# Performance work log

Hardware: AMD Instinct MI355X
Metric: run time of the kernel (lower is better)

Reference implementation:

```python
import jax, jax.numpy as jnp
import numpy as np

DIM = 96
HEADS = 4
HID = int(DIM * 2.66)  # 255, GDFN hidden width
B, H, W = 4, 128, 128


def _conv(x, w, b=None, groups=1):
    y = jax.lax.conv_general_dilated(x, w, (1, 1), 'SAME',
                                     dimension_numbers=('NCHW', 'OIHW', 'NCHW'),
                                     feature_group_count=groups)
    return y if b is None else y + b[None, :, None, None]


def _ln(x, w, b):
    # WithBias LayerNorm over channel dim (per pixel), biased variance, eps=1e-5
    mu = x.mean(1, keepdims=True)
    var = ((x - mu) ** 2).mean(1, keepdims=True)
    return (x - mu) / jnp.sqrt(var + 1e-5) * w[None, :, None, None] + b[None, :, None, None]


def _l2norm(x):
    # torch F.normalize(dim=-1): x / max(||x||_2, 1e-12)
    return x / jnp.maximum(jnp.linalg.norm(x, axis=-1, keepdims=True), 1e-12)


def _gelu(x):
    return jax.nn.gelu(x, approximate=False)


def setup_inputs() -> dict:
    key = jax.random.key(0)
    ks = iter(jax.random.split(key, 32))
    nrm = lambda shp, s=0.02: jax.random.normal(next(ks), shp, dtype=jnp.float32) * s
    d, h2 = DIM, HID
    inp = {
        'x': jax.random.normal(next(ks), (B, DIM, H, W), dtype=jnp.float32),
        # L_conv: 3x3(d->d,+b) GELU 1x1(d->1,+b)
        'Lc_w1': nrm((d, d, 3, 3)), 'Lc_b1': jnp.zeros((d,), jnp.float32),
        'Lc_w2': nrm((1, d, 1, 1)), 'Lc_b2': jnp.zeros((1,), jnp.float32),
        # R_conv: 3x3(d->d,+b) GELU 1x1(d->3,+b)
        'Rc_w1': nrm((d, d, 3, 3)), 'Rc_b1': jnp.zeros((d,), jnp.float32),
        'Rc_w2': nrm((3, d, 1, 1)), 'Rc_b2': jnp.zeros((3,), jnp.float32),
        # L_rein: 3x3(1->d,+b) GELU ; R_rein: 3x3(3->d,+b)
        'Lr_w': nrm((d, 1, 3, 3)), 'Lr_b': jnp.zeros((d,), jnp.float32),
        'Rr_w': nrm((d, 3, 3, 3)), 'Rr_b': jnp.zeros((d,), jnp.float32),
        # LayerNorms (WithBias)
        'n1_w': jnp.ones((d,), jnp.float32), 'n1_b': jnp.zeros((d,), jnp.float32),
        'nL_w': jnp.ones((d,), jnp.float32), 'nL_b': jnp.zeros((d,), jnp.float32),
        'n2_w': jnp.ones((d,), jnp.float32), 'n2_b': jnp.zeros((d,), jnp.float32),
        # Illum_Attention (bias=False)
        'temp': jnp.ones((HEADS, 1, 1), jnp.float32),
        'q_w': nrm((d, d, 1, 1)),
        'qd_w': nrm((d, d, 3, 3)),          # q_dwconv is a FULL 3x3 conv (no groups)
        'kv_w': nrm((2 * d, d, 1, 1)),
        'kvd_w': nrm((2 * d, 1, 3, 3)),     # depthwise, groups=2*dim
        'po_w': nrm((d, d, 1, 1)),
        # FeedForward (bias=False); NOTE: 'dwconv' here is a FULL 3x3 conv
        'pi_w': nrm((h2, d, 1, 1)),
        'fdw_w': nrm((h2, h2, 3, 3)),
        'fpo_w': nrm((d, h2, 1, 1)),
    }
    return inp


def reference(x, Lc_w1, Lc_b1, Lc_w2, Lc_b2, Rc_w1, Rc_b1, Rc_w2, Rc_b2,
              Lr_w, Lr_b, Rr_w, Rr_b, n1_w, n1_b, nL_w, nL_b, n2_w, n2_b,
              temp, q_w, qd_w, kv_w, kvd_w, po_w, pi_w, fdw_w, fpo_w):
    b, c, h, w = x.shape
    # Retinex decomposition heads
    L = _conv(_gelu(_conv(x, Lc_w1, Lc_b1)), Lc_w2, Lc_b2)   # [b,1,h,w]
    R = _conv(_gelu(_conv(x, Rc_w1, Rc_b1)), Rc_w2, Rc_b2)   # [b,3,h,w]
    L_rein = _gelu(_conv(jax.lax.stop_gradient(L), Lr_w, Lr_b))  # detach in torch
    R_rein = _conv(jax.lax.stop_gradient(R), Rr_w, Rr_b)
    # Illum_Guided_TransformerBlock: x = x + attn(norm1(x), normL(illum))
    xn = _ln(x, n1_w, n1_b)
    ill = _ln(L_rein, nL_w, nL_b)
    q = _conv(_conv(ill, q_w), qd_w)
    kv = _conv(_conv(xn, kv_w), kvd_w, groups=2 * c)
    k, v = jnp.split(kv, 2, axis=1)
    ch, hw = c // HEADS, h * w
    heads = lambda t: t.reshape(b, HEADS, ch, hw)
    qh, kh, vh = _l2norm(heads(q)), _l2norm(heads(k)), heads(v)
    # channel-wise attention: [b,heads,ch,ch]
    attn = jax.nn.softmax(jnp.einsum('bhci,bhdi->bhcd', qh, kh) * temp[None], axis=-1)
    out = jnp.einsum('bhcd,bhdi->bhci', attn, vh).reshape(b, c, h, w)
    x = x + _conv(out, po_w)
    # x = x + ffn(norm2(x))
    x2 = _ln(x, n2_w, n2_b)
    x = x + _conv(_gelu(_conv(_conv(x2, pi_w), fdw_w)), fpo_w)
    x = x + R_rein
    return (x, L, R)
```

## Files before the change

### kernel.cpp

```cpp
#include <hip/hip_runtime.h>

#define HWsz 16384
#define Wd 128

typedef unsigned short ushortT;
typedef unsigned int uintT;
typedef __attribute__((ext_vector_type(8))) short short8v;
typedef __attribute__((ext_vector_type(4))) float f32x4;
typedef __attribute__((ext_vector_type(16))) float f32x16;
typedef __attribute__((ext_vector_type(4))) unsigned short ushort4v;

__device__ __forceinline__ float gelu_f(float x){
    return 0.5f * x * (1.0f + erff(x * 0.70710678118654752f));
}
__device__ __forceinline__ ushortT f2b(float f){
    union { float f; uintT u; } v; v.f = f;
    uintT r = v.u + 0x7FFFu + ((v.u >> 16) & 1u);
    return (ushortT)(r >> 16);
}
__device__ __forceinline__ float b2f(ushortT u){
    union { uintT u; float f; } v; v.u = ((uintT)u) << 16; return v.f;
}

__device__ __forceinline__ void pack3_one(int e, const float* __restrict__ w,
    ushortT* __restrict__ outp, int cout, int cin, int BN, int NCH)
{
    int j = e & 7; int r = e >> 3;
    int ocl = r % BN; r /= BN;
    int kg  = r & 3;  r >>= 2;
    int tap = r % 9;  r /= 9;
    int ch  = r % NCH;
    int nt  = r / NCH;
    int ci = ch*32 + kg*8 + j;
    int oc = nt*BN + ocl;
    float v = (oc < cout && ci < cin) ? w[((size_t)oc*cin + ci)*9 + tap] : 0.f;
    outp[e] = f2b(v);
}
__device__ __forceinline__ void pack1_one(int e, const float* __restrict__ w,
    ushortT* __restrict__ outp, int cout, int cin, int BN, int NCH)
{
    int j = e & 7; int r = e >> 3;
    int ocl = r % BN; r /= BN;
    int kg  = r & 3;  r >>= 2;
    int ch  = r % NCH;
    int nt  = r / NCH;
    int ci = ch*32 + kg*8 + j;
    int oc = nt*BN + ocl;
    float v = (oc < cout && ci < cin) ? w[(size_t)oc*cin + ci] : 0.f;
    outp[e] = f2b(v);
}
__global__ __launch_bounds__(256) void pack_all_kernel(
    const float* Lc, const float* Rc, const float* Qd, const float* Fd,
    const float* Q1, const float* KV1, const float* PI1, const float* FPO1,
    ushortT* dL, ushortT* dR, ushortT* dQ, ushortT* dF,
    ushortT* dq0, ushortT* dkv, ushortT* dpi, ushortT* dfpo)
{
    int e = blockIdx.x*256 + threadIdx.x;
    if      (e < 82944)  pack3_one(e,        Lc, dL, 96, 96, 48, 3);
    else if (e < 165888) pack3_one(e-82944,  Rc, dR, 96, 96, 48, 3);
    else if (e < 248832) pack3_one(e-165888, Qd, dQ, 96, 96, 32, 3);
    else if (e < 838656) pack3_one(e-248832, Fd, dF, 255,255, 64, 8);
    else if (e < 847872) pack1_one(e-838656, Q1, dq0, 96, 96, 96, 3);
    else if (e < 866304) pack1_one(e-847872, KV1,dkv, 192,96, 48, 3);
    else if (e < 890880) pack1_one(e-866304, PI1,dpi, 255,96, 64, 3);
    else if (e < 915456) pack1_one(e-890880, FPO1,dfpo,96,255, 96, 8);
}

__global__ __launch_bounds__(256) void tonhwc_kernel(
    const float* __restrict__ in, ushortT* __restrict__ outp)
{
    const int p = blockIdx.x*256 + threadIdx.x;
    const int b = blockIdx.y;
    const float* ip = in + (size_t)b*96*HWsz + p;
    ushortT* op = outp + ((size_t)b*HWsz + p)*96;
#pragma unroll
    for (int g=0; g<12; g++){
        float v[8];
#pragma unroll
        for (int c=0;c<8;c++) v[c] = ip[(size_t)(g*8+c)*HWsz];
        uint4 pk;
        pk.x = (uintT)f2b(v[0]) | ((uintT)f2b(v[1])<<16);
        pk.y = (uintT)f2b(v[2]) | ((uintT)f2b(v[3])<<16);
        pk.z = (uintT)f2b(v[4]) | ((uintT)f2b(v[5])<<16);
        pk.w = (uintT)f2b(v[6]) | ((uintT)f2b(v[7])<<16);
        *(uint4*)(op + g*8) = pk;
    }
}

template<int NG, int NCH, int ACT, int TWOOUT>
__global__ __launch_bounds__(256,3) void conv3x3_v3(
    const ushortT* __restrict__ inh,
    const ushortT* __restrict__ wpk1, const ushortT* __restrict__ wpk2,
    const float* __restrict__ bias1, const float* __restrict__ bias2,
    ushortT* __restrict__ out1, ushortT* __restrict__ out2,
    int cout, int ocpad)
{
    constexpr int BN = NG*16;
    constexpr int Cpad = NCH*32;
    constexpr int WCH = 9*4*BN*8;
    __shared__ __align__(16) ushortT As[4*180*8];
    __shared__ __align__(16) ushortT Ws[WCH];

    const int tid = threadIdx.x;
    const int l   = tid & 63;
    const int wv  = tid >> 6;
    const int l15 = l & 15;
    const int kg  = l >> 4;
    const int tix = blockIdx.x & 7, tiy = blockIdx.x >> 3;
    const int b   = blockIdx.z;
    const int x0 = tix*16, y0 = tiy*8;

    int nt = blockIdx.y;
    const ushortT* wpk; const float* bias; ushortT* outp; int ntw;
    if (TWOOUT && nt >= 2){ wpk = wpk2; bias = bias2; outp = out2; ntw = nt-2; }
    else { wpk = wpk1; bias = bias1; outp = out1; ntw = nt; }
    const int ocbase = ntw*BN;

    f32x4 acc[2][NG];
#pragma unroll
    for (int m=0;m<2;m++)
#pragma unroll
        for (int n=0;n<NG;n++) acc[m][n] = (f32x4){0.f,0.f,0.f,0.f};

    const ushortT* inb = inh + (size_t)b*HWsz*Cpad;

    for (int ch=0; ch<NCH; ch++){
        __syncthreads();
        if (tid < 180){
            int hy = tid/18, hx = tid - hy*18;
            int gy = y0 + hy - 1, gx = x0 + hx - 1;
            bool ok = ((unsigned)gy < 128u) && ((unsigned)gx < 128u);
#pragma unroll
            for (int g=0; g<4; g++){
                uint4 v; v.x=0u; v.y=0u; v.z=0u; v.w=0u;
                if (ok) v = *(const uint4*)(inb + (size_t)(gy*Wd+gx)*Cpad + ch*32 + g*8);
                *(uint4*)(As + (g*180+tid)*8) = v;
            }
        }
        {
            const uint4* wsrc = (const uint4*)(wpk + ((size_t)ntw*NCH + ch)*WCH);
            uint4* wdst = (uint4*)Ws;
            for (int t=tid; t<WCH/8; t+=256) wdst[t] = wsrc[t];
        }
        __syncthreads();
#pragma unroll
        for (int tp=0; tp<9; tp++){
            const int dy = tp/3, dx = tp - dy*3;
            short8v bf[NG];
#pragma unroll
            for (int n=0;n<NG;n++)
                bf[n] = *(const short8v*)(Ws + ((size_t)(tp*4 + kg)*BN + n*16 + l15)*8);
#pragma unroll
            for (int mg=0;mg<2;mg++){
                short8v a = *(const short8v*)(As + (kg*180 + (wv*2+mg+dy)*18 + l15+dx)*8);
#pragma unroll
                for (int n=0;n<NG;n++)
                    acc[mg][n] = __builtin_amdgcn_mfma_f32_16x16x32_bf16(a, bf[n], acc[mg][n], 0,0,0);
            }
        }
    }
    __syncthreads();
    ushortT* Ts = As + wv*1024;
#pragma unroll
    for (int mg=0;mg<2;mg++){
        int gy = y0 + wv*2 + mg;
        ushortT* orow = outp + ((size_t)b*HWsz + gy*Wd + x0)*ocpad + ocbase;
#pragma unroll
        for (int n=0;n<NG;n++){
            int ocl = n*16 + l15;
            int oc  = ocbase + ocl;
            float bs = (bias && oc < cout) ? bias[oc] : 0.f;
#pragma unroll
            for (int j=0;j<4;j++){
                int pxj = kg*4 + j;
                float r = 0.f;
                if (oc < cout){ r = acc[mg][n][j] + bs; if (ACT) r = gelu_f(r); }
                int seg = ((ocl>>3) + pxj) & 7;
                Ts[pxj*64 + seg*8 + (ocl&7)] = f2b(r);
            }
        }
#pragma unroll
        for (int ps=0; ps < (BN+31)/32; ps++){
            int rpx = l & 15;
            int rs  = (l>>4) + ps*4;
            if (rs*8 < BN){
                int pseg = (rs + rpx) & 7;
                short8v v = *(const short8v*)(Ts + rpx*64 + pseg*8);
                *(short8v*)(orow + (size_t)rpx*ocpad + rs*8) = v;
            }
        }
    }
}

template<int NGW, int NCH>
__global__ __launch_bounds__(256) void gemm1x1_v2(
    const ushortT* __restrict__ inh, const ushortT* __restrict__ wpk,
    ushortT* __restrict__ outp, int cout, int ocpad)
{
    constexpr int BN = NGW*16;
    constexpr int Cpad = NCH*32;
    __shared__ __align__(16) ushortT Ts[4*16*64];

    const int tid = threadIdx.x;
    const int l = tid & 63, wv = tid >> 6, l15 = l & 15, kg = l >> 4;
    const int p0 = blockIdx.x*64;
    const int b  = blockIdx.z;
    const int nt = wv, ocbase = wv*BN;
    const ushortT* inb = inh + (size_t)b*HWsz*Cpad;

    f32x4 acc[4][NGW];
#pragma unroll
    for (int m=0;m<4;m++)
#pragma unroll
        for (int n=0;n<NGW;n++) acc[m][n] = (f32x4){0.f,0.f,0.f,0.f};

#pragma unroll
    for (int ch=0; ch<NCH; ch++){
        short8v a[4], bw[NGW];
#pragma unroll
        for (int mg=0; mg<4; mg++)
            a[mg] = *(const short8v*)(inb + (size_t)(p0 + mg*16 + l15)*Cpad + ch*32 + kg*8);
#pragma unroll
        for (int n=0;n<NGW;n++)
            bw[n] = *(const short8v*)(wpk + (((size_t)(nt*NCH + ch)*4 + kg)*BN + n*16 + l15)*8);
#pragma unroll
        for (int mg=0;mg<4;mg++)
#pragma unroll
            for (int n=0;n<NGW;n++)
                acc[mg][n] = __builtin_amdgcn_mfma_f32_16x16x32_bf16(a[mg], bw[n], acc[mg][n], 0,0,0);
    }
    ushortT* Tw = Ts + wv*1024;
#pragma unroll
    for (int mg=0;mg<4;mg++){
        ushortT* orow = outp + ((size_t)b*HWsz + p0 + mg*16)*ocpad + ocbase;
#pragma unroll
        for (int n=0;n<NGW;n++){
            int ocl = n*16 + l15;
            int oc  = ocbase + ocl;
#pragma unroll
            for (int j=0;j<4;j++){
                int pxj = kg*4 + j;
                float r = (oc < cout) ? acc[mg][n][j] : 0.f;
                int seg = ((ocl>>3) + pxj) & 7;
                Tw[pxj*64 + seg*8 + (ocl&7)] = f2b(r);
            }
        }
#pragma unroll
        for (int ps=0; ps < (BN+31)/32; ps++){
            int rpx = l & 15;
            int rs  = (l>>4) + ps*4;
            if (rs*8 < BN){
                int pseg = (rs + rpx) & 7;
                short8v v = *(const short8v*)(Tw + rpx*64 + pseg*8);
                *(short8v*)(orow + (size_t)rpx*ocpad + rs*8) = v;
            }
        }
    }
}

template<int NG, int NCH, int ACT, int OMODE, int NSPLIT, int XMAP>
__global__ __launch_bounds__(256,4) void conv3x3_mfma(
    const ushortT* __restrict__ inh,
    const ushortT* __restrict__ wpk1, const ushortT* __restrict__ wpk2,
    const float* __restrict__ bias1, const float* __restrict__ bias2,
    void* __restrict__ out1, void* __restrict__ out2,
    int cout, int ocpad)
{
    constexpr int BN = NG*16;
    constexpr int Cpad = NCH*32;
    __shared__ __align__(16) ushortT As[4*324*8];

    const int tid = threadIdx.x;
    const int l   = tid & 63;
    const int wv  = tid >> 6;
    const int l15 = l & 15;
    const int kg  = l >> 4;
    int tile = blockIdx.x, nt = blockIdx.y, b = blockIdx.z;
    const int tix = tile & 7, tiy = tile >> 3;

    const ushortT* wpk = wpk1; const float* bias = bias1; void* outv = out1;
    if (NSPLIT > 0 && nt >= NSPLIT){ nt -= NSPLIT; wpk = wpk2; bias = bias2; outv = out2; }

    f32x4 acc[4][NG];
#pragma unroll
    for (int m=0;m<4;m++)
#pragma unroll
        for (int n=0;n<NG;n++) acc[m][n] = (f32x4){0.f,0.f,0.f,0.f};

    const ushortT* inb = inh + (size_t)b*HWsz*Cpad;

    for (int ch=0; ch<NCH; ch++){
        __syncthreads();
#pragma unroll
        for (int g=0; g<4; g++){
            for (int p=tid; p<324; p+=256){
                int hy = p/18, hx = p - hy*18;
                int gy = tiy*16 + hy - 1, gx = tix*16 + hx - 1;
                uint4 v; v.x=0u; v.y=0u; v.z=0u; v.w=0u;
                if ((unsigned)gy < 128u && (unsigned)gx < 128u)
                    v = *(const uint4*)(inb + (size_t)(gy*Wd+gx)*Cpad + ch*32 + g*8);
                *(uint4*)(As + (g*324+p)*8) = v;
            }
        }
        __syncthreads();
        const ushortT* wch = wpk + (size_t)(nt*NCH + ch)*(9*4*BN*8);
#pragma unroll
        for (int tp=0; tp<9; tp++){
            const int dy = tp/3, dx = tp - dy*3;
            short8v a[4], bf[NG];
#pragma unroll
            for (int mg=0; mg<4; mg++){
                int p = (wv*4 + mg + dy)*18 + l15 + dx;
                a[mg] = *(const short8v*)(As + (kg*324 + p)*8);
            }
#pragma unroll
            for (int n=0;n<NG;n++)
                bf[n] = *(const short8v*)(wch + ((size_t)(tp*4 + kg)*BN + n*16 + l15)*8);
#pragma unroll
            for (int mg=0;mg<4;mg++)
#pragma unroll
                for (int n=0;n<NG;n++)
                    acc[mg][n] = __builtin_amdgcn_mfma_f32_16x16x32_bf16(a[mg], bf[n], acc[mg][n], 0,0,0);
        }
    }
    if (OMODE == 2){
        ushortT* out = (ushortT*)outv;
#pragma unroll
        for (int n=0;n<NG;n++){
            int oc = nt*BN + n*16 + l15;
            if (oc < cout){
                float bs = bias ? bias[oc] : 0.f;
#pragma unroll
                for (int mg=0;mg<4;mg++){
                    int gy = tiy*16 + wv*4 + mg;
                    int gx = tix*16 + kg*4;
                    ushort4v pk;
#pragma unroll
                    for (int j=0;j<4;j++){
                        float r = acc[mg][n][j] + bs;
                        if (ACT) r = gelu_f(r);
                        pk[j] = f2b(r);
                    }
                    *(ushort4v*)(out + ((size_t)b*cout + oc)*HWsz + gy*Wd + gx) = pk;
                }
            }
        }
    }
}

template<int NG, int NCH, int RES, int OMODE, int XMAP>
__global__ __launch_bounds__(256) void gemm1x1_mfma(
    const ushortT* __restrict__ inh, const ushortT* __restrict__ wpk, int wstride_z,
    const float* __restrict__ res1, const ushortT* __restrict__ res2b,
    void* __restrict__ outv, int cout, int ocpad)
{
    constexpr int BN = NG*16;
    constexpr int Cpad = NCH*32;
    constexpr int LSTR = (BN <= 64) ? 64 : 128;
    constexpr int MASK = LSTR/8 - 1;
    __shared__ __align__(16) ushortT TsS[(OMODE==1) ? 4*16*LSTR : 16];

    const int tid = threadIdx.x;
    const int l = tid & 63, wv = tid >> 6, l15 = l & 15, kg = l >> 4;
    int chunk = blockIdx.x, nt = blockIdx.y, b = blockIdx.z;
    const int p0 = chunk*256 + wv*64;
    const ushortT* inb = inh + (size_t)b*HWsz*Cpad;
    const ushortT* wp  = wpk + (size_t)b*wstride_z;

    f32x4 acc[4][NG];
#pragma unroll
    for (int m=0;m<4;m++)
#pragma unroll
        for (int n=0;n<NG;n++) acc[m][n] = (f32x4){0.f,0.f,0.f,0.f};

#pragma unroll
    for (int ch=0; ch<NCH; ch++){
        short8v a[4], bw[NG];
#pragma unroll
        for (int mg=0; mg<4; mg++)
            a[mg] = *(const short8v*)(inb + (size_t)(p0 + mg*16 + l15)*Cpad + ch*32 + kg*8);
#pragma unroll
        for (int n=0;n<NG;n++)
            bw[n] = *(const short8v*)(wp + (((size_t)(nt*NCH + ch)*4 + kg)*BN + n*16 + l15)*8);
#pragma unroll
        for (int mg=0;mg<4;mg++)
#pragma unroll
            for (int n=0;n<NG;n++)
                acc[mg][n] = __builtin_amdgcn_mfma_f32_16x16x32_bf16(a[mg], bw[n], acc[mg][n], 0,0,0);
    }
    if (OMODE == 0){
        float* out = (float*)outv;
#pragma unroll
        for (int n=0;n<NG;n++){
            int oc = nt*BN + n*16 + l15;
            if (oc < cout){
#pragma unroll
                for (int mg=0;mg<4;mg++){
                    int pix = p0 + mg*16 + kg*4;
                    size_t idx = ((size_t)b*cout + oc)*HWsz + pix;
                    float4 r;
                    r.x = acc[mg][n][0]; r.y = acc[mg][n][1];
                    r.z = acc[mg][n][2]; r.w = acc[mg][n][3];
                    if (RES>=1){ float4 q = *(const float4*)(res1+idx); r.x+=q.x;r.y+=q.y;r.z+=q.z;r.w+=q.w; }
                    if (RES>=2){
                        ushort4v q = *(const ushort4v*)(res2b+idx);
                        r.x+=b2f(q[0]); r.y+=b2f(q[1]); r.z+=b2f(q[2]); r.w+=b2f(q[3]);
                    }
                    *(float4*)(out + idx) = r;
                }
            }
        }
    } else {
        ushortT* outp = (ushortT*)outv;
        ushortT* Ts = TsS + wv*(16*LSTR);
#pragma unroll
        for (int mg=0;mg<4;mg++){
            ushortT* orow = outp + ((size_t)b*HWsz + p0 + mg*16)*ocpad + nt*BN;
#pragma unroll
            for (int n=0;n<NG;n++){
                int ocl = n*16 + l15;
                int oc  = nt*BN + ocl;
#pragma unroll
                for (int j=0;j<4;j++){
                    int pxj = kg*4 + j;
                    float r = (oc < cout) ? acc[mg][n][j] : 0.f;
                    int seg = ((ocl>>3) + pxj) & MASK;
                    Ts[pxj*LSTR + seg*8 + (ocl&7)] = f2b(r);
                }
            }
#pragma unroll
            for (int ps=0; ps < (BN+31)/32; ps++){
                int rpx = l & 15;
                int rs  = (l>>4) + ps*4;
                if (rs*8 < BN){
                    int pseg = (rs + rpx) & MASK;
                    short8v v = *(const short8v*)(Ts + rpx*LSTR + pseg*8);
                    *(short8v*)(orow + (size_t)rpx*ocpad + rs*8) = v;
                }
            }
        }
    }
}

template<int NOUT>
__global__ __launch_bounds__(256) void head1x1_kernel(
    const ushortT* __restrict__ inh, const float* __restrict__ w,
    const float* __restrict__ bias, float* __restrict__ out)
{
    __shared__ float lw[NOUT*96];
    const int tid = threadIdx.x;
    for (int t=tid; t<NOUT*96; t+=256) lw[t] = w[t];
    __syncthreads();
    const int p = blockIdx.x*256 + tid;
    const int b = blockIdx.y;
    const ushortT* ip = inh + ((size_t)b*HWsz + p)*96;
    float v[96];
#pragma unroll
    for (int g=0; g<12; g++){
        short8v s = *(const short8v*)(ip + g*8);
#pragma unroll
        for (int i=0;i<8;i++) v[g*8+i] = b2f((ushortT)s[i]);
    }
#pragma unroll
    for (int oc=0; oc<NOUT; oc++){
        float acc = bias[oc];
#pragma unroll
        for (int c=0;c<96;c++) acc += v[c]*lw[oc*96+c];
        out[((size_t)b*NOUT + oc)*HWsz + p] = acc;
    }
}

__global__ __launch_bounds__(256) void lrein_ln_kernel(
    const float* __restrict__ L, const float* __restrict__ w,
    const float* __restrict__ bias, const float* __restrict__ lnw,
    const float* __restrict__ lnb, ushortT* __restrict__ outh)
{
    __shared__ float sw[864], sb[96], sn1[96], sn2[96];
    const int tid = threadIdx.x;
    for (int t=tid; t<864; t+=256) sw[t] = w[t];
    if (tid < 96){ sb[tid]=bias[tid]; sn1[tid]=lnw[tid]; sn2[tid]=lnb[tid]; }
    __syncthreads();
    const int p = blockIdx.x*256 + tid;
    const int b = blockIdx.y;
    const int y = p>>7, x = p&127;
    const float* ib = L + (size_t)b*HWsz;
    float win[9];
#pragma unroll
    for (int dy=0;dy<3;dy++)
#pragma unroll
        for (int dx=0;dx<3;dx++){
            int gy=y+dy-1, gx=x+dx-1;
            win[dy*3+dx] = ((unsigned)gy<128u && (unsigned)gx<128u) ? ib[gy*Wd+gx] : 0.f;
        }
    float v[96]; float s=0.f;
#pragma unroll
    for (int c=0;c<96;c++){
        float a = sb[c];
#pragma unroll
        for (int t=0;t<9;t++) a += win[t]*sw[c*9+t];
        a = gelu_f(a);
        v[c]=a; s+=a;
    }
    const float mu = s*(1.f/96.f);
    float s2=0.f;
#pragma unroll
    for (int c=0;c<96;c++){ float d=v[c]-mu; s2+=d*d; }
    const float inv = 1.f/sqrtf(s2*(1.f/96.f)+1e-5f);
    ushortT* op = outh + ((size_t)b*HWsz + p)*96;
#pragma unroll
    for (int g=0; g<12; g++){
        uint4 pk; uintT w4[4];
#pragma unroll
        for (int i=0;i<4;i++){
            float r0 = (v[g*8+2*i]-mu)*inv*sn1[g*8+2*i]+sn2[g*8+2*i];
            float r1 = (v[g*8+2*i+1]-mu)*inv*sn1[g*8+2*i+1]+sn2[g*8+2*i+1];
            w4[i] = (uintT)f2b(r0) | ((uintT)f2b(r1)<<16);
        }
        pk.x=w4[0]; pk.y=w4[1]; pk.z=w4[2]; pk.w=w4[3];
        *(uint4*)(op + g*8) = pk;
    }
}

__global__ __launch_bounds__(256) void ln_n2n_kernel(
    const float* __restrict__ in, const float* __restrict__ w,
    const float* __restrict__ bias, ushortT* __restrict__ outh)
{
    const int p = blockIdx.x*256+threadIdx.x;
    const int b = blockIdx.y;
    const float* ip = in + (size_t)b*96*HWsz + p;
    float v[96]; float s=0.f;
#pragma unroll
    for(int c=0;c<96;c++){ v[c]=ip[(size_t)c*HWsz]; s+=v[c]; }
    const float mu = s*(1.f/96.f);
    float s2=0.f;
#pragma unroll
    for(int c=0;c<96;c++){ float d=v[c]-mu; s2+=d*d; }
    const float inv = 1.f/sqrtf(s2*(1.f/96.f)+1e-5f);
    ushortT* op = outh + ((size_t)b*HWsz + p)*96;
#pragma unroll
    for (int g=0; g<12; g++){
        uint4 pk; uintT w4[4];
#pragma unroll
        for (int i=0;i<4;i++){
            float r0 = (v[g*8+2*i]-mu)*inv*w[g*8+2*i]+bias[g*8+2*i];
            float r1 = (v[g*8+2*i+1]-mu)*inv*w[g*8+2*i+1]+bias[g*8+2*i+1];
            w4[i] = (uintT)f2b(r0) | ((uintT)f2b(r1)<<16);
        }
        pk.x=w4[0]; pk.y=w4[1]; pk.z=w4[2]; pk.w=w4[3];
        *(uint4*)(op + g*8) = pk;
    }
}

__global__ __launch_bounds__(256) void conv3x3_rr_kernel(
    const float* __restrict__ in, const float* __restrict__ w,
    const float* __restrict__ bias, ushortT* __restrict__ out)
{
    __shared__ float sw[216], sb[8];
    const int oc0 = blockIdx.y*8;
    if (threadIdx.x < 216) sw[threadIdx.x] = w[(size_t)oc0*27 + threadIdx.x];
    if (threadIdx.x < 8)   sb[threadIdx.x] = bias[oc0 + threadIdx.x];
    __syncthreads();
    const int p = blockIdx.x*256+threadIdx.x;
    const int b = blockIdx.z;
    const int y=p>>7, x=p&127;
    const float* ib = in + (size_t)b*3*HWsz;
    float win[27];
#pragma unroll
    for (int ci=0;ci<3;ci++)
#pragma unroll
        for (int dy=0;dy<3;dy++)
#pragma unroll
            for (int dx=0;dx<3;dx++){
                int gy=y+dy-1, gx=x+dx-1;
                win[ci*9+dy*3+dx] = ((unsigned)gy<128u && (unsigned)gx<128u)
                    ? ib[(size_t)ci*HWsz + gy*Wd+gx] : 0.f;
            }
#pragma unroll
    for (int i=0;i<8;i++){
        float acc = sb[i];
#pragma unroll
        for (int t=0;t<27;t++) acc += win[t]*sw[i*27+t];
        out[((size_t)b*96 + oc0+i)*HWsz + p] = f2b(acc);
    }
}

__global__ __launch_bounds__(256) void dw_nhwc_kernel(
    const ushortT* __restrict__ inh, const float* __restrict__ w,
    ushortT* __restrict__ kout, ushortT* __restrict__ vouth)
{
    const int p = blockIdx.x*256+threadIdx.x;
    const int c0 = blockIdx.y*8;
    const int b = blockIdx.z;
    const int y=p>>7, x=p&127;
    float lw[72];
#pragma unroll
    for (int i=0;i<8;i++)
#pragma unroll
        for (int t=0;t<9;t++) lw[i*9+t] = w[(size_t)(c0+i)*9 + t];
    const ushortT* ib = inh + (size_t)b*HWsz*192;
    float acc[8];
#pragma unroll
    for (int i=0;i<8;i++) acc[i]=0.f;
#pragma unroll
    for(int dy=0;dy<3;dy++){
        int gy=y+dy-1;
        if((unsigned)gy<128u){
#pragma unroll
            for(int dx=0;dx<3;dx++){
                int gx=x+dx-1;
                if((unsigned)gx<128u){
                    short8v s = *(const short8v*)(ib + (size_t)(gy*Wd+gx)*192 + c0);
#pragma unroll
                    for (int i=0;i<8;i++) acc[i] += b2f((ushortT)s[i])*lw[i*9+dy*3+dx];
                }
            }
        }
    }
    if (c0 < 96){
#pragma unroll
        for (int i=0;i<8;i++)
            kout[((size_t)b*96 + c0+i)*HWsz + p] = f2b(acc[i]);
    } else {
        ushortT* op = vouth + ((size_t)b*HWsz + p)*96 + (c0-96);
        uint4 pk;
        pk.x = (uintT)f2b(acc[0]) | ((uintT)f2b(acc[1])<<16);
        pk.y = (uintT)f2b(acc[2]) | ((uintT)f2b(acc[3])<<16);
        pk.z = (uintT)f2b(acc[4]) | ((uintT)f2b(acc[5])<<16);
        pk.w = (uintT)f2b(acc[6]) | ((uintT)f2b(acc[7])<<16);
        *(uint4*)op = pk;
    }
}

__global__ __launch_bounds__(256) void rownorm_bf16_kernel(
    const ushortT* __restrict__ qb, const ushortT* __restrict__ kb,
    float* __restrict__ invqk)
{
    __shared__ float red[256];
    const int r = blockIdx.x;
    const ushortT* ip = (r < 384) ? (qb + (size_t)r*HWsz) : (kb + (size_t)(r-384)*HWsz);
    float s=0.f;
    const ushortT* tp = ip + threadIdx.x*64;
#pragma unroll
    for (int g=0; g<8; g++){
        short8v v = *(const short8v*)(tp + g*8);
#pragma unroll
        for (int i=0;i<8;i++){ float f = b2f((ushortT)v[i]); s += f*f; }
    }
    red[threadIdx.x]=s; __syncthreads();
    for(int st=128; st>0; st>>=1){
        if(threadIdx.x<st) red[threadIdx.x]+=red[threadIdx.x+st];
        __syncthreads();
    }
    if(threadIdx.x==0) invqk[r] = 1.f/fmaxf(sqrtf(red[0]), 1e-12f);
}

__global__ __launch_bounds__(256) void qk_mfma_kernel(
    const ushortT* __restrict__ qb, const ushortT* __restrict__ kb,
    float* __restrict__ part)
{
    const int tid = threadIdx.x;
    const int l = tid & 63, wv = tid >> 6;
    const int chunk = blockIdx.x*4 + wv;
    const int bh = blockIdx.y, b = bh>>2, h = bh&3;
    const int ch = min(l & 31, 23);
    const int kh = (l >> 5)*8;
    const ushortT* qp = qb + ((size_t)b*96 + h*24 + ch)*HWsz + chunk*512 + kh;
    const ushortT* kp = kb + ((size_t)b*96 + h*24 + ch)*HWsz + chunk*512 + kh;
    f32x16 acc;
#pragma unroll
    for (int r=0;r<16;r++) acc[r]=0.f;
    for (int ks=0; ks<32; ks++){
        short8v a  = *(const short8v*)(qp + ks*16);
        short8v bb = *(const short8v*)(kp + ks*16);
        acc = __builtin_amdgcn_mfma_f32_32x32x16_bf16(a, bb, acc, 0,0,0);
    }
    float* op = part + ((size_t)chunk*16 + bh)*1024;
    const int col = l & 31;
#pragma unroll
    for (int r=0;r<16;r++){
        int row = (r&3) + 8*(r>>2) + 4*(l>>5);
        op[row*32 + col] = acc[r];
    }
}

__global__ void qk_reduce_kernel(const float* __restrict__ part, float* __restrict__ out)
{
    int idx = blockIdx.x*256+threadIdx.x;
    float s=0.f;
    for(int c=0;c<32;c++) s += part[(size_t)c*16384 + idx];
    out[idx]=s;
}

__global__ __launch_bounds__(576) void softmax_kernel(
    const float* __restrict__ raw, const float* __restrict__ invq,
    const float* __restrict__ invk, const float* __restrict__ temp,
    float* __restrict__ attn)
{
    __shared__ float l[576];
    const int bh=blockIdx.x, b=bh>>2, h=bh&3;
    const int tid=threadIdx.x;
    const int i=tid/24, j=tid-i*24;
    l[tid] = raw[(size_t)bh*1024 + i*32 + j] * invq[b*96+h*24+i] * invk[b*96+h*24+j] * temp[h];
    __syncthreads();
    if(tid<24){
        float m=-1e30f;
#pragma unroll
        for(int jj=0;jj<24;jj++) m = fmaxf(m, l[tid*24+jj]);
        float e[24]; float s=0.f;
#pragma unroll
        for(int jj=0;jj<24;jj++){ e[jj]=__expf(l[tid*24+jj]-m); s+=e[jj]; }
        float isv = 1.f/s;
#pragma unroll
        for(int jj=0;jj<24;jj++) attn[(size_t)bh*576 + tid*24 + jj] = e[jj]*isv;
    }
}

__global__ __launch_bounds__(256) void mkM_kernel(
    const float* __restrict__ attn, const float* __restrict__ po_w,
    ushortT* __restrict__ Mpk)
{
    const int b = blockIdx.x;
    for (int e = threadIdx.x; e < 9216; e += 256){
        int oc = e / 96, d = e - oc*96;
        int h = d / 24, dl = d - h*24;
        const float* aw = attn + ((size_t)(b*4+h))*576 + dl;
        const float* pw = po_w + (size_t)oc*96 + h*24;
        float s = 0.f;
#pragma unroll
        for (int c=0;c<24;c++) s += pw[c]*aw[c*24];
        int ch = d>>5, kg = (d>>3)&3, j = d&7;
        Mpk[(size_t)b*9216 + ((size_t)(ch*4+kg)*96 + oc)*8 + j] = f2b(s);
    }
}

extern "C" void kernel_launch(void* const* d_in, const int* in_sizes, int n_in,
                              void* d_out, int out_size, void* d_ws, size_t ws_size,
                              hipStream_t stream)
{
    const float* x     = (const float*)d_in[0];
    const float* Lc_w1 = (const float*)d_in[1];
    const float* Lc_b1 = (const float*)d_in[2];
    const float* Lc_w2 = (const float*)d_in[3];
    const float* Lc_b2 = (const float*)d_in[4];
    const float* Rc_w1 = (const float*)d_in[5];
    const float* Rc_b1 = (const float*)d_in[6];
    const float* Rc_w2 = (const float*)d_in[7];
    const float* Rc_b2 = (const float*)d_in[8];
    const float* Lr_w  = (const float*)d_in[9];
    const float* Lr_b  = (const float*)d_in[10];
    const float* Rr_w  = (const float*)d_in[11];
    const float* Rr_b  = (const float*)d_in[12];
    const float* n1_w  = (const float*)d_in[13];
    const float* n1_b  = (const float*)d_in[14];
    const float* nL_w  = (const float*)d_in[15];
    const float* nL_b  = (const float*)d_in[16];
    const float* n2_w  = (const float*)d_in[17];
    const float* n2_b  = (const float*)d_in[18];
    const float* temp  = (const float*)d_in[19];
    const float* q_w   = (const float*)d_in[20];
    const float* qd_w  = (const float*)d_in[21];
    const float* kv_w  = (const float*)d_in[22];
    const float* kvd_w = (const float*)d_in[23];
    const float* po_w  = (const float*)d_in[24];
    const float* pi_w  = (const float*)d_in[25];
    const float* fdw_w = (const float*)d_in[26];
    const float* fpo_w = (const float*)d_in[27];

    char* base = (char*)d_ws;
    ushortT* xh   = (ushortT*)(base + 0);
    ushortT* f0h  = (ushortT*)(base + 0);
    ushortT* Lh   = (ushortT*)(base + 33554432);
    ushortT* kv0h = (ushortT*)(base + 33554432);
    ushortT* f1h  = (ushortT*)(base + 33554432);
    ushortT* Rh   = (ushortT*)(base + 67108864);
    ushortT* vh   = (ushortT*)(base + 67108864);
    ushortT* x2nh = (ushortT*)(base + 67108864);
    ushortT* illh = (ushortT*)(base + 79691776);
    ushortT* xnh  = (ushortT*)(base + 92274688);
    ushortT* q0h  = (ushortT*)(base + 104857600);
    ushortT* qb   = (ushortT*)(base + 117440512);
    float*   x1   = (float*)(base + 117440512);
    ushortT* kb   = (ushortT*)(base + 142606336);
    ushortT* Bb   = (ushortT*)(base + 155189248);
    char* smb = base + 167772160;
    ushortT* wpkL = (ushortT*)smb;   smb += 165888;
    ushortT* wpkR = (ushortT*)smb;   smb += 165888;
    ushortT* wpkQ = (ushortT*)smb;   smb += 165888;
    ushortT* wpkF = (ushortT*)smb;   smb += 1179648;
    ushortT* wq0  = (ushortT*)smb;   smb += 18432;
    ushortT* wkv  = (ushortT*)smb;   smb += 36864;
    ushortT* wpi  = (ushortT*)smb;   smb += 49152;
    ushortT* wfpo = (ushortT*)smb;   smb += 49152;
    ushortT* Mpk  = (ushortT*)smb;   smb += 73728;
    float* invqk  = (float*)smb;     smb += 3072;
    float* part   = (float*)smb;     smb += 2097152;
    float* araw   = (float*)smb;     smb += 65536;
    float* attn   = (float*)smb;     smb += 36864;

    float* out_x = (float*)d_out;
    float* out_L = out_x + (size_t)4*96*HWsz;
    float* out_R = out_L + (size_t)4*HWsz;

    dim3 blk(256);

    hipLaunchKernelGGL(pack_all_kernel, dim3(3576), blk, 0, stream,
        Lc_w1, Rc_w1, qd_w, fdw_w, q_w, kv_w, pi_w, fpo_w,
        wpkL, wpkR, wpkQ, wpkF, wq0, wkv, wpi, wfpo);
    hipLaunchKernelGGL(tonhwc_kernel, dim3(64,4), blk, 0, stream, x, xh);

    hipLaunchKernelGGL((conv3x3_v3<3,3,1,1>), dim3(128,4,4), blk, 0, stream,
        xh, wpkL, wpkR, Lc_b1, Rc_b1, Lh, Rh, 96, 96);
    hipLaunchKernelGGL((head1x1_kernel<1>), dim3(64,4), blk, 0, stream, Lh, Lc_w2, Lc_b2, out_L);
    hipLaunchKernelGGL((head1x1_kernel<3>), dim3(64,4), blk, 0, stream, Rh, Rc_w2, Rc_b2, out_R);
    hipLaunchKernelGGL(lrein_ln_kernel, dim3(64,4), blk, 0, stream, out_L, Lr_w, Lr_b, nL_w, nL_b, illh);
    hipLaunchKernelGGL(conv3x3_rr_kernel, dim3(64,12,4), blk, 0, stream, out_R, Rr_w, Rr_b, Bb);

    hipLaunchKernelGGL(ln_n2n_kernel, dim3(64,4), blk, 0, stream, x, n1_w, n1_b, xnh);

    hipLaunchKernelGGL((gemm1x1_mfma<6,3,0,1,0>), dim3(64,1,4), blk, 0, stream,
        illh, wq0, 0, nullptr, nullptr, (void*)q0h, 96, 96);
    hipLaunchKernelGGL((conv3x3_mfma<2,3,0,2,0,0>), dim3(64,3,4), blk, 0, stream,
        q0h, wpkQ, wpkQ, nullptr, nullptr, (void*)qb, (void*)qb, 96, 0);
    hipLaunchKernelGGL((gemm1x1_v2<3,3>), dim3(256,1,4), blk, 0, stream,
        xnh, wkv, kv0h, 192, 192);
    hipLaunchKernelGGL(dw_nhwc_kernel, dim3(64,24,4), blk, 0, stream, kv0h, kvd_w, kb, vh);

    hipLaunchKernelGGL(rownorm_bf16_kernel, dim3(768), blk, 0, stream, qb, kb, invqk);
    hipLaunchKernelGGL(qk_mfma_kernel, dim3(8,16), blk, 0, stream, qb, kb, part);
    hipLaunchKernelGGL(qk_reduce_kernel, dim3(64), blk, 0, stream, part, araw);
    hipLaunchKernelGGL(softmax_kernel, dim3(16), dim3(576), 0, stream, araw, invqk, invqk+384, temp, attn);
    hipLaunchKernelGGL(mkM_kernel, dim3(4), blk, 0, stream, attn, po_w, Mpk);
    hipLaunchKernelGGL((gemm1x1_mfma<6,3,1,0,0>), dim3(64,1,4), blk, 0, stream,
        vh, Mpk, 9216, x, nullptr, (void*)x1, 96, 0);

    hipLaunchKernelGGL(ln_n2n_kernel, dim3(64,4), blk, 0, stream, x1, n2_w, n2_b, x2nh);
    hipLaunchKernelGGL((gemm1x1_v2<4,3>), dim3(256,1,4), blk, 0, stream,
        x2nh, wpi, f0h, 255, 256);
    hipLaunchKernelGGL((conv3x3_v3<4,8,1,0>), dim3(128,4,4), blk, 0, stream,
        f0h, wpkF, wpkF, nullptr, nullptr, f1h, f1h, 255, 256);
    hipLaunchKernelGGL((gemm1x1_mfma<6,8,2,0,0>), dim3(64,1,4), blk, 0, stream,
        f1h, wfpo, 0, x1, Bb, (void*)out_x, 96, 0);
}
```

Measured before the change: 408.6 us.

## Double conv3x3 spatial tile height and load weights via direct global-to-LDS

```diff
diff --git a/kernel.cpp b/kernel.cpp
--- a/kernel.cpp
+++ b/kernel.cpp
@@ -20,6 +20,11 @@
 }
 __device__ __forceinline__ float b2f(ushortT u){
     union { uintT u; float f; } v; v.u = ((uintT)u) << 16; return v.f;
+}
+__device__ __forceinline__ void gload_lds16(const ushortT* g, ushortT* l){
+    __builtin_amdgcn_global_load_lds(
+        (const __attribute__((address_space(1))) void*)g,
+        (__attribute__((address_space(3))) void*)l, 16, 0, 0);
 }
 
 __device__ __forceinline__ void pack3_one(int e, const float* __restrict__ w,
@@ -88,7 +93,7 @@
 }
 
 template<int NG, int NCH, int ACT, int TWOOUT>
-__global__ __launch_bounds__(256,3) void conv3x3_v3(
+__global__ __launch_bounds__(256,2) void conv3x3_v4(
     const ushortT* __restrict__ inh,
     const ushortT* __restrict__ wpk1, const ushortT* __restrict__ wpk2,
     const float* __restrict__ bias1, const float* __restrict__ bias2,
@@ -97,9 +102,10 @@
 {
     constexpr int BN = NG*16;
     constexpr int Cpad = NCH*32;
-    constexpr int WCH = 9*4*BN*8;
-    __shared__ __align__(16) ushortT As[4*180*8];
-    __shared__ __align__(16) ushortT Ws[WCH];
+    constexpr int WCH4 = 9*4*BN;
+    constexpr int WI = (WCH4 + 255)/256;
+    __shared__ __align__(16) ushortT As[4*324*8];
+    __shared__ __align__(16) ushortT Ws[WCH4*8];
 
     const int tid = threadIdx.x;
     const int l   = tid & 63;
@@ -108,7 +114,7 @@
     const int kg  = l >> 4;
     const int tix = blockIdx.x & 7, tiy = blockIdx.x >> 3;
     const int b   = blockIdx.z;
-    const int x0 = tix*16, y0 = tiy*8;
+    const int x0 = tix*16, y0 = tiy*16;
 
     int nt = blockIdx.y;
     const ushortT* wpk; const float* bias; ushortT* outp; int ntw;
@@ -116,9 +122,9 @@
     else { wpk = wpk1; bias = bias1; outp = out1; ntw = nt; }
     const int ocbase = ntw*BN;
 
-    f32x4 acc[2][NG];
-#pragma unroll
-    for (int m=0;m<2;m++)
+    f32x4 acc[4][NG];
+#pragma unroll
+    for (int m=0;m<4;m++)
 #pragma unroll
         for (int n=0;n<NG;n++) acc[m][n] = (f32x4){0.f,0.f,0.f,0.f};
 
@@ -126,21 +132,23 @@
 
     for (int ch=0; ch<NCH; ch++){
         __syncthreads();
-        if (tid < 180){
-            int hy = tid/18, hx = tid - hy*18;
+        for (int t=tid; t<1296; t+=256){
+            int p = t>>2, g = t&3;
+            int hy = p/18, hx = p - hy*18;
             int gy = y0 + hy - 1, gx = x0 + hx - 1;
-            bool ok = ((unsigned)gy < 128u) && ((unsigned)gx < 128u);
-#pragma unroll
-            for (int g=0; g<4; g++){
-                uint4 v; v.x=0u; v.y=0u; v.z=0u; v.w=0u;
-                if (ok) v = *(const uint4*)(inb + (size_t)(gy*Wd+gx)*Cpad + ch*32 + g*8);
-                *(uint4*)(As + (g*180+tid)*8) = v;
-            }
+            uint4 v; v.x=0u; v.y=0u; v.z=0u; v.w=0u;
+            if ((unsigned)gy < 128u && (unsigned)gx < 128u)
+                v = *(const uint4*)(inb + (size_t)(gy*Wd+gx)*Cpad + ch*32 + g*8);
+            *(uint4*)(As + (g*324+p)*8) = v;
         }
         {
-            const uint4* wsrc = (const uint4*)(wpk + ((size_t)ntw*NCH + ch)*WCH);
-            uint4* wdst = (uint4*)Ws;
-            for (int t=tid; t<WCH/8; t+=256) wdst[t] = wsrc[t];
+            const ushortT* wsrc = wpk + ((size_t)ntw*NCH + ch)*(WCH4*8);
+#pragma unroll
+            for (int i=0; i<WI; i++){
+                int t = i*256 + tid;
+                if ((WCH4 & 255) == 0 || t < WCH4)
+                    gload_lds16(wsrc + (size_t)t*8, Ws + (size_t)t*8);
+            }
         }
         __syncthreads();
 #pragma unroll
@@ -151,8 +159,8 @@
             for (int n=0;n<NG;n++)
                 bf[n] = *(const short8v*)(Ws + ((size_t)(tp*4 + kg)*BN + n*16 + l15)*8);
 #pragma unroll
-            for (int mg=0;mg<2;mg++){
-                short8v a = *(const short8v*)(As + (kg*180 + (wv*2+mg+dy)*18 + l15+dx)*8);
+            for (int mg=0;mg<4;mg++){
+                short8v a = *(const short8v*)(As + (kg*324 + (wv*4+mg+dy)*18 + l15+dx)*8);
 #pragma unroll
                 for (int n=0;n<NG;n++)
                     acc[mg][n] = __builtin_amdgcn_mfma_f32_16x16x32_bf16(a, bf[n], acc[mg][n], 0,0,0);
@@ -162,8 +170,8 @@
     __syncthreads();
     ushortT* Ts = As + wv*1024;
 #pragma unroll
-    for (int mg=0;mg<2;mg++){
-        int gy = y0 + wv*2 + mg;
+    for (int mg=0;mg<4;mg++){
+        int gy = y0 + wv*4 + mg;
         ushortT* orow = outp + ((size_t)b*HWsz + gy*Wd + x0)*ocpad + ocbase;
 #pragma unroll
         for (int n=0;n<NG;n++){
@@ -808,7 +816,7 @@
         wpkL, wpkR, wpkQ, wpkF, wq0, wkv, wpi, wfpo);
     hipLaunchKernelGGL(tonhwc_kernel, dim3(64,4), blk, 0, stream, x, xh);
 
-    hipLaunchKernelGGL((conv3x3_v3<3,3,1,1>), dim3(128,4,4), blk, 0, stream,
+    hipLaunchKernelGGL((conv3x3_v4<3,3,1,1>), dim3(64,4,4), blk, 0, stream,
         xh, wpkL, wpkR, Lc_b1, Rc_b1, Lh, Rh, 96, 96);
     hipLaunchKernelGGL((head1x1_kernel<1>), dim3(64,4), blk, 0, stream, Lh, Lc_w2, Lc_b2, out_L);
     hipLaunchKernelGGL((head1x1_kernel<3>), dim3(64,4), blk, 0, stream, Rh, Rc_w2, Rc_b2, out_R);
@@ -836,7 +844,7 @@
     hipLaunchKernelGGL(ln_n2n_kernel, dim3(64,4), blk, 0, stream, x1, n2_w, n2_b, x2nh);
     hipLaunchKernelGGL((gemm1x1_v2<4,3>), dim3(256,1,4), blk, 0, stream,
         x2nh, wpi, f0h, 255, 256);
-    hipLaunchKernelGGL((conv3x3_v3<4,8,1,0>), dim3(128,4,4), blk, 0, stream,
+    hipLaunchKernelGGL((conv3x3_v4<4,8,1,0>), dim3(64,4,4), blk, 0, stream,
         f0h, wpkF, wpkF, nullptr, nullptr, f1h, f1h, 255, 256);
     hipLaunchKernelGGL((gemm1x1_mfma<6,8,2,0,0>), dim3(64,1,4), blk, 0, stream,
         f1h, wfpo, 0, x1, Bb, (void*)out_x, 96, 0);
```

After: 376.9 us. -7.8%, faster.
